# Kernel optimization log

Measured on AMD Instinct MI355X. Metric: run time of the kernel, lower is better.

Reference implementation:

```python
import jax, jax.numpy as jnp
import numpy as np

EPS_BN = 1e-5
NEG_SLOPE = 0.2

def _bn(x, gamma, beta):
    # BatchNorm1d using batch statistics (training-mode math, biased var as torch)
    mu = jnp.mean(x, axis=0)
    var = jnp.var(x, axis=0)
    return (x - mu) * jax.lax.rsqrt(var + EPS_BN) * gamma + beta

def _gat(x, src, dst, W, att_src, att_dst, bias, N):
    # x: [N, Fin]; W: [Fin, H*C]; att_*: [H, C]
    H, C = att_src.shape
    h = (x @ W).reshape(N, H, C)                       # [N,H,C]
    a_src = jnp.sum(h * att_src, axis=-1)              # [N,H]
    a_dst = jnp.sum(h * att_dst, axis=-1)              # [N,H]
    alpha = jax.nn.leaky_relu(a_src[src] + a_dst[dst], NEG_SLOPE)  # [E,H]
    # segment softmax over destination nodes
    m = jax.ops.segment_max(alpha, dst, num_segments=N)           # [N,H]
    e = jnp.exp(alpha - m[dst])
    s = jax.ops.segment_sum(e, dst, num_segments=N)
    a = e / (s[dst] + 1e-16)                           # [E,H]
    msg = h[src] * a[:, :, None]                       # [E,H,C]
    out = jax.ops.segment_sum(msg, dst, num_segments=N)  # [N,H,C]
    return out.reshape(N, H * C) + bias

def setup_inputs() -> dict:
    key = jax.random.key(0)
    ks = jax.random.split(key, 16)
    N, Fin, Hid = 50000, 128, 64
    E = 800000
    x = jax.random.normal(ks[0], (N, Fin), dtype=jnp.float32)
    edge_index = jax.random.randint(ks[1], (2, E), 0, N, dtype=jnp.int32)
    sc = 0.1
    return {
        'x': x,
        'edge_index': edge_index,
        'W1': jax.random.normal(ks[2], (Fin, 2 * Hid), jnp.float32) * sc,
        'att_src1': jax.random.normal(ks[3], (2, Hid), jnp.float32) * sc,
        'att_dst1': jax.random.normal(ks[4], (2, Hid), jnp.float32) * sc,
        'b1': jnp.zeros((2 * Hid,), jnp.float32),
        'g1': jnp.ones((2 * Hid,), jnp.float32),
        'be1': jnp.zeros((2 * Hid,), jnp.float32),
        'W2': jax.random.normal(ks[5], (2 * Hid, Hid), jnp.float32) * sc,
        'att_src2': jax.random.normal(ks[6], (1, Hid), jnp.float32) * sc,
        'att_dst2': jax.random.normal(ks[7], (1, Hid), jnp.float32) * sc,
        'b2': jnp.zeros((Hid,), jnp.float32),
        'g2': jnp.ones((Hid,), jnp.float32),
        'be2': jnp.zeros((Hid,), jnp.float32),
        'linW': jax.random.normal(ks[8], (Hid, 1), jnp.float32) * sc,
        'linb': jnp.zeros((1,), jnp.float32),
    }

def reference(x, edge_index, W1, att_src1, att_dst1, b1, g1, be1,
              W2, att_src2, att_dst2, b2, g2, be2, linW, linb):
    N = x.shape[0]
    loops = jnp.arange(N, dtype=edge_index.dtype)
    src = jnp.concatenate([edge_index[0], loops])  # PyG adds self-loops
    dst = jnp.concatenate([edge_index[1], loops])
    h = _gat(x, src, dst, W1, att_src1, att_dst1, b1, N)
    h = jax.nn.relu(_bn(h, g1, be1))                 # dropout = identity (eval)
    h = _gat(h, src, dst, W2, att_src2, att_dst2, b2, N)
    h = jax.nn.relu(_bn(h, g2, be2))
    return (h @ linW + linb).squeeze(-1)
```

## Files before the change

kernel.cpp:

```cpp
#include <hip/hip_runtime.h>
#include <hip/hip_fp16.h>
#include <math.h>

#define LEAKY 0.2f
#define XPAD 136
#define MAXB 512

typedef _Float16 f16x8 __attribute__((ext_vector_type(8)));
typedef float f32x4 __attribute__((ext_vector_type(4)));

__device__ inline int h2i(__half2 h) { union { __half2 h; int i; } u; u.h = h; return u.i; }
__device__ inline __half2 i2h(int i) { union { __half2 h; int i; } u; u.i = i; return u.h; }

__global__ __launch_bounds__(256) void k_bhist(const int* __restrict__ ei,
                                               int* __restrict__ gbcnt, int E, int PB)
{
  __shared__ int lh[MAXB];
  int t = threadIdx.x;
  for (int i = t; i < PB; i += 256) lh[i] = 0;
  __syncthreads();
  int base = blockIdx.x * 2048;
#pragma unroll
  for (int k = 0; k < 8; ++k) {
    int idx = base + t + k * 256;
    if (idx < E) atomicAdd(&lh[ei[E + idx] >> 7], 1);
  }
  __syncthreads();
  for (int i = t; i < PB; i += 256) if (lh[i]) atomicAdd(&gbcnt[i], lh[i]);
}

__global__ __launch_bounds__(512) void k_bscan(const int* __restrict__ gbcnt,
                                               int* __restrict__ pbase,
                                               int* __restrict__ gcur, int PB)
{
  __shared__ int ls[512];
  int t = threadIdx.x;
  int v = (t < PB) ? gbcnt[t] : 0;
  ls[t] = v;
  __syncthreads();
  for (int off = 1; off < 512; off <<= 1) {
    int u = (t >= off) ? ls[t - off] : 0;
    __syncthreads();
    ls[t] += u;
    __syncthreads();
  }
  int excl = ls[t] - v;
  if (t <= PB) pbase[t] = excl;
  if (t < PB) gcur[t] = excl;
}

__global__ __launch_bounds__(256) void k_part(const int* __restrict__ ei,
                                              int* __restrict__ gcur,
                                              int2* __restrict__ pairs, int E, int PB)
{
  __shared__ int lcnt[MAXB], lbase[MAXB];
  int t = threadIdx.x;
  for (int i = t; i < PB; i += 256) lcnt[i] = 0;
  __syncthreads();
  int base = blockIdx.x * 4096;
  int lsrc[16], ldst[16], lp[16];
#pragma unroll
  for (int k = 0; k < 16; ++k) {
    int idx = base + t + k * 256;
    lp[k] = -1;
    if (idx < E) {
      int s = ei[idx], d = ei[E + idx];
      lsrc[k] = s; ldst[k] = d;
      int b = d >> 7;
      int p = atomicAdd(&lcnt[b], 1);
      lp[k] = (p << 10) | b;
    }
  }
  __syncthreads();
  for (int b = t; b < PB; b += 256) lbase[b] = atomicAdd(&gcur[b], lcnt[b]);
  __syncthreads();
#pragma unroll
  for (int k = 0; k < 16; ++k) {
    if (lp[k] >= 0) {
      int b = lp[k] & 1023, p = lp[k] >> 10;
      pairs[lbase[b] + p] = make_int2(lsrc[k], ldst[k]);
    }
  }
}

__global__ __launch_bounds__(256) void k_fine(const int2* __restrict__ pairs,
                                              const int* __restrict__ pbase,
                                              int* __restrict__ rowptr,
                                              int* __restrict__ colx, int N)
{
  __shared__ int ldeg[128], lcur[128];
  int b = blockIdx.x, t = threadIdx.x;
  int nbase = b << 7;
  int nbn = N - nbase; if (nbn > 128) nbn = 128;
  if (t < 128) ldeg[t] = (t < nbn) ? 1 : 0;
  __syncthreads();
  int e0 = pbase[b], e1 = pbase[b + 1];
  for (int e = e0 + t; e < e1; e += 256) atomicAdd(&ldeg[pairs[e].y - nbase], 1);
  __syncthreads();
  int myv = (t < 128) ? ldeg[t] : 0;
  for (int off = 1; off < 128; off <<= 1) {
    int u = (t < 128 && t >= off) ? ldeg[t - off] : 0;
    __syncthreads();
    if (t < 128) ldeg[t] += u;
    __syncthreads();
  }
  int colx0 = e0 + nbase;
  if (t < 128) {
    int excl = ldeg[t] - myv;
    lcur[t] = colx0 + excl;
    int idx = nbase + t;
    if (idx <= N) rowptr[idx] = colx0 + excl;
  }
  __syncthreads();
  for (int e = e0 + t; e < e1; e += 256) {
    int2 p = pairs[e];
    int pos = atomicAdd(&lcur[p.y - nbase], 1);
    colx[pos] = p.x;
  }
  if (t < nbn) {
    int pos = atomicAdd(&lcur[t], 1);
    colx[pos] = nbase + t;
  }
}

__global__ __launch_bounds__(256) void k_gemm1(
    const float* __restrict__ x, const float* __restrict__ W,
    const float* __restrict__ att_s, const float* __restrict__ att_d,
    unsigned* __restrict__ h1h, float* __restrict__ a1s, float* __restrict__ a1d, int N)
{
  __shared__ __align__(16) _Float16 Xh[64 * XPAD];
  __shared__ __align__(16) _Float16 Wt[128 * XPAD];
  int t = threadIdx.x;
  const float4* W4 = (const float4*)W;
#pragma unroll
  for (int i = 0; i < 16; ++i) {
    int id = t + i * 256;
    int row = id >> 5, c0 = (id & 31) * 4;
    float4 wv = W4[id];
    Wt[(c0    ) * XPAD + row] = (_Float16)wv.x;
    Wt[(c0 + 1) * XPAD + row] = (_Float16)wv.y;
    Wt[(c0 + 2) * XPAD + row] = (_Float16)wv.z;
    Wt[(c0 + 3) * XPAD + row] = (_Float16)wv.w;
  }
  int row0 = blockIdx.x * 64;
  const float4* X4 = (const float4*)x;
#pragma unroll
  for (int i = 0; i < 8; ++i) {
    int id = t + i * 256;
    int r = id >> 5, c = id & 31;
    int gr = row0 + r;
    float4 v = (gr < N) ? X4[(size_t)gr * 32 + c] : make_float4(0.f, 0.f, 0.f, 0.f);
    unsigned p01 = (unsigned)h2i(__floats2half2_rn(v.x, v.y));
    unsigned p23 = (unsigned)h2i(__floats2half2_rn(v.z, v.w));
    *(uint2*)&Xh[r * XPAD + c * 4] = make_uint2(p01, p23);
  }
  __syncthreads();
  int w = t >> 6, l = t & 63;
  int m = l & 15, kg = l >> 4;
  f32x4 acc[8];
#pragma unroll
  for (int c = 0; c < 8; ++c) { acc[c][0] = 0.f; acc[c][1] = 0.f; acc[c][2] = 0.f; acc[c][3] = 0.f; }
#pragma unroll
  for (int ks = 0; ks < 4; ++ks) {
    f16x8 a = *(const f16x8*)&Xh[(w * 16 + m) * XPAD + ks * 32 + kg * 8];
#pragma unroll
    for (int c = 0; c < 8; ++c) {
      f16x8 bfr = *(const f16x8*)&Wt[(c * 16 + m) * XPAD + ks * 32 + kg * 8];
      acc[c] = __builtin_amdgcn_mfma_f32_16x16x32_f16(a, bfr, acc[c], 0, 0, 0);
    }
  }
#pragma unroll
  for (int c = 0; c < 8; ++c)
#pragma unroll
    for (int r = 0; r < 4; ++r)
      Xh[(w * 16 + kg * 4 + r) * XPAD + c * 16 + m] = (_Float16)acc[c][r];
  __syncthreads();
#pragma unroll
  for (int i = 0; i < 8; ++i) {
    int id = t + i * 256;
    int r = id >> 5, c4 = id & 31;
    int gr = row0 + r;
    uint2 pk = *(const uint2*)&Xh[r * XPAD + c4 * 4];
    float2 v01 = __half22float2(i2h((int)pk.x));
    float2 v23 = __half22float2(i2h((int)pk.y));
    int col = c4 * 4;
    float4 asv = *(const float4*)&att_s[col];
    float4 adv = *(const float4*)&att_d[col];
    float ps = v01.x * asv.x + v01.y * asv.y + v23.x * asv.z + v23.y * asv.w;
    float pd = v01.x * adv.x + v01.y * adv.y + v23.x * adv.z + v23.y * adv.w;
    ps += __shfl_xor(ps, 1); ps += __shfl_xor(ps, 2); ps += __shfl_xor(ps, 4); ps += __shfl_xor(ps, 8);
    pd += __shfl_xor(pd, 1); pd += __shfl_xor(pd, 2); pd += __shfl_xor(pd, 4); pd += __shfl_xor(pd, 8);
    if (gr < N) {
      *(uint2*)&h1h[(size_t)gr * 64 + c4 * 2] = pk;
      if ((t & 15) == 0) { int h = (t >> 4) & 1; a1s[gr * 2 + h] = ps; a1d[gr * 2 + h] = pd; }
    }
  }
}

__global__ __launch_bounds__(256) void k_agg1(
    const int* __restrict__ rowptr, const int* __restrict__ colx,
    const unsigned* __restrict__ h1h, const float* __restrict__ a1s,
    const float* __restrict__ a1d, const float* __restrict__ b1,
    unsigned* __restrict__ v1h, float* __restrict__ stats, int N)
{
  int t = threadIdx.x;
  int w = t >> 6, lane = t & 63;
  int g = lane >> 4, q = lane & 15;
  bool hi = q >= 8;
  int n = blockIdx.x * 16 + w * 4 + g;
  bool act = n < N;
  float4 biasA = *(const float4*)&b1[q * 8];
  float4 biasB = *(const float4*)&b1[q * 8 + 4];
  int start = 0, end = 0;
  float2 ad = make_float2(0.f, 0.f);
  if (act) { start = rowptr[n]; end = rowptr[n + 1]; ad = *(const float2*)&a1d[n * 2]; }
  float se = 0.f;
  float4 accA = {0, 0, 0, 0}, accB = {0, 0, 0, 0};
  for (int base = start; base < end; base += 16) {
    int cnt = end - base; if (cnt > 16) cnt = 16;
    int sl = 0, epk = 0;
    if (q < cnt) {
      sl = colx[base + q];
      float2 av = *(const float2*)&a1s[sl * 2];
      float x0 = av.x + ad.x, x1 = av.y + ad.y;
      x0 = (x0 > 0.f) ? x0 : LEAKY * x0;
      x1 = (x1 > 0.f) ? x1 : LEAKY * x1;
      epk = h2i(__floats2half2_rn(__expf(x0), __expf(x1)));
    }
    int j = 0;
    if (cnt == 16) {
      int ss[16], ee[16];
#pragma unroll
      for (int k = 0; k < 16; ++k) { ss[k] = __shfl(sl, k, 16); ee[k] = __shfl(epk, k, 16); }
      uint4 rr[16];
#pragma unroll
      for (int k = 0; k < 16; ++k) rr[k] = *(const uint4*)&h1h[(size_t)ss[k] * 64 + q * 4];
#pragma unroll
      for (int k = 0; k < 16; ++k) {
        float2 ef = __half22float2(i2h(ee[k]));
        float wg = hi ? ef.y : ef.x;
        float2 r0 = __half22float2(i2h((int)rr[k].x));
        float2 r1 = __half22float2(i2h((int)rr[k].y));
        float2 r2 = __half22float2(i2h((int)rr[k].z));
        float2 r3 = __half22float2(i2h((int)rr[k].w));
        se += wg;
        accA.x = fmaf(wg, r0.x, accA.x); accA.y = fmaf(wg, r0.y, accA.y);
        accA.z = fmaf(wg, r1.x, accA.z); accA.w = fmaf(wg, r1.y, accA.w);
        accB.x = fmaf(wg, r2.x, accB.x); accB.y = fmaf(wg, r2.y, accB.y);
        accB.z = fmaf(wg, r3.x, accB.z); accB.w = fmaf(wg, r3.y, accB.w);
      }
      j = 16;
    }
    int lim8 = cnt & ~7;
    for (; j < lim8; j += 8) {
      int ss[8], ee[8];
#pragma unroll
      for (int k = 0; k < 8; ++k) { ss[k] = __shfl(sl, j + k, 16); ee[k] = __shfl(epk, j + k, 16); }
      uint4 rr[8];
#pragma unroll
      for (int k = 0; k < 8; ++k) rr[k] = *(const uint4*)&h1h[(size_t)ss[k] * 64 + q * 4];
#pragma unroll
      for (int k = 0; k < 8; ++k) {
        float2 ef = __half22float2(i2h(ee[k]));
        float wg = hi ? ef.y : ef.x;
        float2 r0 = __half22float2(i2h((int)rr[k].x));
        float2 r1 = __half22float2(i2h((int)rr[k].y));
        float2 r2 = __half22float2(i2h((int)rr[k].z));
        float2 r3 = __half22float2(i2h((int)rr[k].w));
        se += wg;
        accA.x = fmaf(wg, r0.x, accA.x); accA.y = fmaf(wg, r0.y, accA.y);
        accA.z = fmaf(wg, r1.x, accA.z); accA.w = fmaf(wg, r1.y, accA.w);
        accB.x = fmaf(wg, r2.x, accB.x); accB.y = fmaf(wg, r2.y, accB.y);
        accB.z = fmaf(wg, r3.x, accB.z); accB.w = fmaf(wg, r3.y, accB.w);
      }
    }
    for (; j < cnt; ++j) {
      int s0 = __shfl(sl, j, 16), e0 = __shfl(epk, j, 16);
      float2 ef = __half22float2(i2h(e0));
      float wg = hi ? ef.y : ef.x;
      uint4 rv = *(const uint4*)&h1h[(size_t)s0 * 64 + q * 4];
      float2 r0 = __half22float2(i2h((int)rv.x));
      float2 r1 = __half22float2(i2h((int)rv.y));
      float2 r2 = __half22float2(i2h((int)rv.z));
      float2 r3 = __half22float2(i2h((int)rv.w));
      se += wg;
      accA.x = fmaf(wg, r0.x, accA.x); accA.y = fmaf(wg, r0.y, accA.y);
      accA.z = fmaf(wg, r1.x, accA.z); accA.w = fmaf(wg, r1.y, accA.w);
      accB.x = fmaf(wg, r2.x, accB.x); accB.y = fmaf(wg, r2.y, accB.y);
      accB.z = fmaf(wg, r3.x, accB.z); accB.w = fmaf(wg, r3.y, accB.w);
    }
  }
  float4 oA = {0,0,0,0}, oB = {0,0,0,0};
  if (act) {
    float inv = 1.f / se;
    oA.x = fmaf(accA.x, inv, biasA.x);
    oA.y = fmaf(accA.y, inv, biasA.y);
    oA.z = fmaf(accA.z, inv, biasA.z);
    oA.w = fmaf(accA.w, inv, biasA.w);
    oB.x = fmaf(accB.x, inv, biasB.x);
    oB.y = fmaf(accB.y, inv, biasB.y);
    oB.z = fmaf(accB.z, inv, biasB.z);
    oB.w = fmaf(accB.w, inv, biasB.w);
    unsigned p0 = (unsigned)h2i(__floats2half2_rn(oA.x, oA.y));
    unsigned p1 = (unsigned)h2i(__floats2half2_rn(oA.z, oA.w));
    unsigned p2 = (unsigned)h2i(__floats2half2_rn(oB.x, oB.y));
    unsigned p3 = (unsigned)h2i(__floats2half2_rn(oB.z, oB.w));
    *(uint4*)&v1h[(size_t)n * 64 + q * 4] = make_uint4(p0, p1, p2, p3);
  }
  __shared__ float redS[4][64][8], redQ[4][64][8];
#pragma unroll
  for (int j2 = 0; j2 < 4; ++j2) {
    redS[w][lane][j2]     = (&oA.x)[j2];
    redS[w][lane][4 + j2] = (&oB.x)[j2];
    redQ[w][lane][j2]     = (&oA.x)[j2] * (&oA.x)[j2];
    redQ[w][lane][4 + j2] = (&oB.x)[j2] * (&oB.x)[j2];
  }
  __syncthreads();
  if (t < 128) {
    int qq = t >> 3, jj = t & 7;
    float s = 0.f, sq = 0.f;
#pragma unroll
    for (int w2 = 0; w2 < 4; ++w2)
#pragma unroll
      for (int g2 = 0; g2 < 4; ++g2) {
        s  += redS[w2][g2 * 16 + qq][jj];
        sq += redQ[w2][g2 * 16 + qq][jj];
      }
    int sl8 = (blockIdx.x & 7) * 256;
    atomicAdd(&stats[sl8 + t], s);
    atomicAdd(&stats[sl8 + 128 + t], sq);
  }
}

__global__ __launch_bounds__(256) void k_gemm2(
    const unsigned* __restrict__ v1h, const float* __restrict__ W2,
    const float* __restrict__ stats, const float* __restrict__ g1, const float* __restrict__ be1,
    const float* __restrict__ att_s, const float* __restrict__ att_d,
    unsigned* __restrict__ h2h, float* __restrict__ a2s, float* __restrict__ a2d,
    int N, float rcpN)
{
  __shared__ __align__(16) _Float16 Xh[64 * XPAD];
  __shared__ __align__(16) _Float16 Wt[64 * XPAD];
  __shared__ float kc[128], sc[128];
  int t = threadIdx.x;
  if (t < 128) {
    float su = 0.f, sq = 0.f;
#pragma unroll
    for (int s8 = 0; s8 < 8; ++s8) { su += stats[s8 * 256 + t]; sq += stats[s8 * 256 + 128 + t]; }
    float mu = su * rcpN;
    float var = sq * rcpN - mu * mu;
    float kk = g1[t] * rsqrtf(var + 1e-5f);
    kc[t] = kk; sc[t] = be1[t] - mu * kk;
  }
  const float4* W4 = (const float4*)W2;
#pragma unroll
  for (int i = 0; i < 8; ++i) {
    int id = t + i * 256;
    int row = id >> 4, c0 = (id & 15) * 4;
    float4 wv = W4[id];
    Wt[(c0    ) * XPAD + row] = (_Float16)wv.x;
    Wt[(c0 + 1) * XPAD + row] = (_Float16)wv.y;
    Wt[(c0 + 2) * XPAD + row] = (_Float16)wv.z;
    Wt[(c0 + 3) * XPAD + row] = (_Float16)wv.w;
  }
  __syncthreads();
  int row0 = blockIdx.x * 64;
#pragma unroll
  for (int i = 0; i < 8; ++i) {
    int id = t + i * 256;
    int r = id >> 5, c4 = id & 31;
    int gr = row0 + r;
    uint2 pv = (gr < N) ? *(const uint2*)&v1h[(size_t)gr * 64 + c4 * 2] : make_uint2(0, 0);
    float2 a01 = __half22float2(i2h((int)pv.x));
    float2 a23 = __half22float2(i2h((int)pv.y));
    int f0 = c4 * 4;
    float o0 = fmaxf(a01.x * kc[f0]     + sc[f0],     0.f);
    float o1 = fmaxf(a01.y * kc[f0 + 1] + sc[f0 + 1], 0.f);
    float o2 = fmaxf(a23.x * kc[f0 + 2] + sc[f0 + 2], 0.f);
    float o3 = fmaxf(a23.y * kc[f0 + 3] + sc[f0 + 3], 0.f);
    unsigned p01 = (unsigned)h2i(__floats2half2_rn(o0, o1));
    unsigned p23 = (unsigned)h2i(__floats2half2_rn(o2, o3));
    *(uint2*)&Xh[r * XPAD + c4 * 4] = make_uint2(p01, p23);
  }
  __syncthreads();
  int w = t >> 6, l = t & 63;
  int m = l & 15, kg = l >> 4;
  f32x4 acc[4];
#pragma unroll
  for (int c = 0; c < 4; ++c) { acc[c][0] = 0.f; acc[c][1] = 0.f; acc[c][2] = 0.f; acc[c][3] = 0.f; }
#pragma unroll
  for (int ks = 0; ks < 4; ++ks) {
    f16x8 a = *(const f16x8*)&Xh[(w * 16 + m) * XPAD + ks * 32 + kg * 8];
#pragma unroll
    for (int c = 0; c < 4; ++c) {
      f16x8 bfr = *(const f16x8*)&Wt[(c * 16 + m) * XPAD + ks * 32 + kg * 8];
      acc[c] = __builtin_amdgcn_mfma_f32_16x16x32_f16(a, bfr, acc[c], 0, 0, 0);
    }
  }
#pragma unroll
  for (int c = 0; c < 4; ++c)
#pragma unroll
    for (int r = 0; r < 4; ++r)
      Xh[(w * 16 + kg * 4 + r) * XPAD + c * 16 + m] = (_Float16)acc[c][r];
  __syncthreads();
#pragma unroll
  for (int i = 0; i < 4; ++i) {
    int id = t + i * 256;
    int r = id >> 4, c4 = id & 15;
    int gr = row0 + r;
    uint2 pk = *(const uint2*)&Xh[r * XPAD + c4 * 4];
    float2 v01 = __half22float2(i2h((int)pk.x));
    float2 v23 = __half22float2(i2h((int)pk.y));
    int col = c4 * 4;
    float4 asv = *(const float4*)&att_s[col];
    float4 adv = *(const float4*)&att_d[col];
    float ps = v01.x * asv.x + v01.y * asv.y + v23.x * asv.z + v23.y * asv.w;
    float pd = v01.x * adv.x + v01.y * adv.y + v23.x * adv.z + v23.y * adv.w;
    ps += __shfl_xor(ps, 1); ps += __shfl_xor(ps, 2); ps += __shfl_xor(ps, 4); ps += __shfl_xor(ps, 8);
    pd += __shfl_xor(pd, 1); pd += __shfl_xor(pd, 2); pd += __shfl_xor(pd, 4); pd += __shfl_xor(pd, 8);
    if (gr < N) {
      *(uint2*)&h2h[(size_t)gr * 32 + c4 * 2] = pk;
      if ((t & 15) == 0) { a2s[gr] = ps; a2d[gr] = pd; }
    }
  }
}

__global__ __launch_bounds__(256) void k_agg2(
    const int* __restrict__ rowptr, const int* __restrict__ colx,
    const unsigned* __restrict__ h2h, const float* __restrict__ a2s,
    const float* __restrict__ a2d, const float* __restrict__ b2,
    unsigned* __restrict__ v2h, float* __restrict__ stats, int N)
{
  int t = threadIdx.x;
  int w = t >> 6, lane = t & 63;
  int g = lane >> 4, q = lane & 15;
  int n = blockIdx.x * 16 + w * 4 + g;
  bool act = n < N;
  float4 bias = *(const float4*)&b2[q * 4];
  int start = 0, end = 0;
  float ad = 0.f;
  if (act) { start = rowptr[n]; end = rowptr[n + 1]; ad = a2d[n]; }
  float se = 0.f;
  float4 acc = {0, 0, 0, 0};
  for (int base = start; base < end; base += 16) {
    int cnt = end - base; if (cnt > 16) cnt = 16;
    int sl = 0; float ev = 0.f;
    if (q < cnt) {
      sl = colx[base + q];
      float av = a2s[sl] + ad;
      av = (av > 0.f) ? av : LEAKY * av;
      ev = __expf(av);
    }
    int j = 0;
    if (cnt == 16) {
      int ss[16]; float ee[16];
#pragma unroll
      for (int k = 0; k < 16; ++k) { ss[k] = __shfl(sl, k, 16); ee[k] = __shfl(ev, k, 16); }
      uint2 rr[16];
#pragma unroll
      for (int k = 0; k < 16; ++k) rr[k] = *(const uint2*)&h2h[(size_t)ss[k] * 32 + q * 2];
#pragma unroll
      for (int k = 0; k < 16; ++k) {
        float2 r01 = __half22float2(i2h((int)rr[k].x));
        float2 r23 = __half22float2(i2h((int)rr[k].y));
        se += ee[k];
        acc.x = fmaf(ee[k], r01.x, acc.x);
        acc.y = fmaf(ee[k], r01.y, acc.y);
        acc.z = fmaf(ee[k], r23.x, acc.z);
        acc.w = fmaf(ee[k], r23.y, acc.w);
      }
      j = 16;
    }
    int lim8 = cnt & ~7;
    for (; j < lim8; j += 8) {
      int ss[8]; float ee[8];
#pragma unroll
      for (int k = 0; k < 8; ++k) { ss[k] = __shfl(sl, j + k, 16); ee[k] = __shfl(ev, j + k, 16); }
      uint2 rr[8];
#pragma unroll
      for (int k = 0; k < 8; ++k) rr[k] = *(const uint2*)&h2h[(size_t)ss[k] * 32 + q * 2];
#pragma unroll
      for (int k = 0; k < 8; ++k) {
        float2 r01 = __half22float2(i2h((int)rr[k].x));
        float2 r23 = __half22float2(i2h((int)rr[k].y));
        se += ee[k];
        acc.x = fmaf(ee[k], r01.x, acc.x);
        acc.y = fmaf(ee[k], r01.y, acc.y);
        acc.z = fmaf(ee[k], r23.x, acc.z);
        acc.w = fmaf(ee[k], r23.y, acc.w);
      }
    }
    for (; j < cnt; ++j) {
      int s0 = __shfl(sl, j, 16);
      float e0 = __shfl(ev, j, 16);
      uint2 rv = *(const uint2*)&h2h[(size_t)s0 * 32 + q * 2];
      float2 r01 = __half22float2(i2h((int)rv.x));
      float2 r23 = __half22float2(i2h((int)rv.y));
      se += e0;
      acc.x = fmaf(e0, r01.x, acc.x);
      acc.y = fmaf(e0, r01.y, acc.y);
      acc.z = fmaf(e0, r23.x, acc.z);
      acc.w = fmaf(e0, r23.y, acc.w);
    }
  }
  float4 o = {0, 0, 0, 0};
  if (act) {
    float inv = 1.f / se;
    o.x = fmaf(acc.x, inv, bias.x);
    o.y = fmaf(acc.y, inv, bias.y);
    o.z = fmaf(acc.z, inv, bias.z);
    o.w = fmaf(acc.w, inv, bias.w);
    unsigned p01 = (unsigned)h2i(__floats2half2_rn(o.x, o.y));
    unsigned p23 = (unsigned)h2i(__floats2half2_rn(o.z, o.w));
    *(uint2*)&v2h[(size_t)n * 32 + q * 2] = make_uint2(p01, p23);
  }
  __shared__ float4 reds[4][64], redq[4][64];
  reds[w][lane] = o;
  redq[w][lane] = make_float4(o.x * o.x, o.y * o.y, o.z * o.z, o.w * o.w);
  __syncthreads();
  if (t < 64) {
    int qq = t >> 2, ii = t & 3;
    float s = 0.f, sq = 0.f;
#pragma unroll
    for (int w2 = 0; w2 < 4; ++w2)
#pragma unroll
      for (int g2 = 0; g2 < 4; ++g2) {
        s  += (&reds[w2][g2 * 16 + qq].x)[ii];
        sq += (&redq[w2][g2 * 16 + qq].x)[ii];
      }
    int sl8 = (blockIdx.x & 7) * 128;
    atomicAdd(&stats[sl8 + t], s);
    atomicAdd(&stats[sl8 + 64 + t], sq);
  }
}

__global__ __launch_bounds__(256) void k_out(
    const unsigned* __restrict__ v2h, const float* __restrict__ stats,
    const float* __restrict__ g2, const float* __restrict__ be2,
    const float* __restrict__ linW, const float* __restrict__ linb,
    float* __restrict__ out, int N, float rcpN)
{
  __shared__ float kc[64], sc[64], lw[64];
  int t = threadIdx.x;
  if (t < 64) {
    float su = 0.f, sq = 0.f;
#pragma unroll
    for (int s8 = 0; s8 < 8; ++s8) { su += stats[s8 * 128 + t]; sq += stats[s8 * 128 + 64 + t]; }
    float mu = su * rcpN;
    float var = sq * rcpN - mu * mu;
    float kk = g2[t] * rsqrtf(var + 1e-5f);
    kc[t] = kk; sc[t] = be2[t] - mu * kk; lw[t] = linW[t];
  }
  __syncthreads();
  int w = t >> 6, lane = t & 63, g = lane >> 5, q = lane & 31;
  int n = blockIdx.x * 8 + w * 2 + g;
  if (n >= N) return;
  unsigned uv = v2h[(size_t)n * 32 + q];
  float2 vf = __half22float2(i2h((int)uv));
  float h0 = fmaxf(vf.x * kc[2 * q] + sc[2 * q], 0.f);
  float h1 = fmaxf(vf.y * kc[2 * q + 1] + sc[2 * q + 1], 0.f);
  float p = fmaf(h0, lw[2 * q], h1 * lw[2 * q + 1]);
#pragma unroll
  for (int off = 16; off; off >>= 1) p += __shfl_xor(p, off, 32);
  if (q == 0) out[n] = p + linb[0];
}

extern "C" void kernel_launch(void* const* d_in, const int* in_sizes, int n_in,
                              void* d_out, int out_size, void* d_ws, size_t ws_size,
                              hipStream_t stream)
{
  const float* x    = (const float*)d_in[0];
  const int*   ei   = (const int*)d_in[1];
  const float* W1   = (const float*)d_in[2];
  const float* as1  = (const float*)d_in[3];
  const float* ad1  = (const float*)d_in[4];
  const float* b1   = (const float*)d_in[5];
  const float* g1   = (const float*)d_in[6];
  const float* be1  = (const float*)d_in[7];
  const float* W2   = (const float*)d_in[8];
  const float* as2  = (const float*)d_in[9];
  const float* ad2  = (const float*)d_in[10];
  const float* b2   = (const float*)d_in[11];
  const float* g2   = (const float*)d_in[12];
  const float* be2  = (const float*)d_in[13];
  const float* linW = (const float*)d_in[14];
  const float* linb = (const float*)d_in[15];
  float* out = (float*)d_out;

  int N = in_sizes[0] / 128;
  int E = in_sizes[1] / 2;
  int Etot = E + N;
  float rcpN = 1.f / (float)N;
  int PB = (N + 127) / 128;

  float* ws = (float*)d_ws;
  size_t o = 0;
  float* H1HF = ws + o; o += (size_t)N * 64;
  float* V1HF = ws + o; o += (size_t)N * 64;
  float* A1S  = ws + o; o += (size_t)N * 2;
  float* A1D  = ws + o; o += (size_t)N * 2;
  float* A2S  = ws + o; o += N;
  float* A2D  = ws + o; o += N;
  float* ST1  = ws + o; o += 8 * 256;
  float* ST2  = ws + o; o += 8 * 128;
  int* GBCNT  = (int*)(ws + o); o += MAXB;
  int* PBASE  = (int*)(ws + o); o += MAXB + 1;
  int* GCUR   = (int*)(ws + o); o += MAXB;
  int* ROWPTR = (int*)(ws + o); o += (size_t)N + 1;
  int* COL    = (int*)(ws + o); o += (size_t)Etot;
  int2* PAIRS = (int2*)(ws + o); o += (size_t)E * 2;
  unsigned* H1H = (unsigned*)H1HF;
  unsigned* H2H = (unsigned*)H1HF;
  unsigned* V1H = (unsigned*)V1HF;
  unsigned* V2H = (unsigned*)V1HF;

  hipMemsetAsync(ST1, 0, (3072 + MAXB) * 4, stream);

  int gb  = (N + 63) / 64;
  int bh  = (E + 2047) / 2048;
  int pt  = (E + 4095) / 4096;
  int ab1 = (N + 15) / 16;
  int ab2 = (N + 15) / 16;
  int ob  = (N + 7) / 8;

  k_bhist<<<bh, 256, 0, stream>>>(ei, GBCNT, E, PB);
  k_bscan<<<1, 512, 0, stream>>>(GBCNT, PBASE, GCUR, PB);
  k_part<<<pt, 256, 0, stream>>>(ei, GCUR, PAIRS, E, PB);
  k_fine<<<PB, 256, 0, stream>>>(PAIRS, PBASE, ROWPTR, COL, N);
  k_gemm1<<<gb, 256, 0, stream>>>(x, W1, as1, ad1, H1H, A1S, A1D, N);
  k_agg1<<<ab1, 256, 0, stream>>>(ROWPTR, COL, H1H, A1S, A1D, b1, V1H, ST1, N);
  k_gemm2<<<gb, 256, 0, stream>>>(V1H, W2, ST1, g1, be1, as2, ad2, H2H, A2S, A2D, N, rcpN);
  k_agg2<<<ab2, 256, 0, stream>>>(ROWPTR, COL, H2H, A2S, A2D, b2, V2H, ST2, N);
  k_out<<<ob, 256, 0, stream>>>(V2H, ST2, g2, be2, linW, linb, out, N, rcpN);
}
```

Before: 167.2 us.

## Fold bucket scan into partition kernels and widen layer-2 aggregation vectors

Removes the single-block k_bscan launch by having every k_part block redundantly scan the bucket counts. k_fine now derives its edge range with a block-level reduction over the preceding counts, and GCUR becomes a zero-based offset cleared by the enlarged memset. k_agg2 switches to 8 lanes per node with 16-byte gathers, 8 channels per lane and 32 nodes per block, and the reduction buffers get padding to avoid LDS bank conflicts. This saves a launch and a serial dependency, but adds redundant scan work in every partition and fine block.

```diff
diff --git a/kernel.cpp b/kernel.cpp
--- a/kernel.cpp
+++ b/kernel.cpp
@@ -29,50 +29,44 @@
   for (int i = t; i < PB; i += 256) if (lh[i]) atomicAdd(&gbcnt[i], lh[i]);
 }
 
-__global__ __launch_bounds__(512) void k_bscan(const int* __restrict__ gbcnt,
-                                               int* __restrict__ pbase,
-                                               int* __restrict__ gcur, int PB)
-{
-  __shared__ int ls[512];
+__global__ __launch_bounds__(256) void k_part(const int* __restrict__ ei,
+                                              const int* __restrict__ gbcnt,
+                                              int* __restrict__ gcur,
+                                              int2* __restrict__ pairs, int E, int PB)
+{
+  __shared__ int lcnt[MAXB], lpb[MAXB], lbase[MAXB], ls[256];
   int t = threadIdx.x;
-  int v = (t < PB) ? gbcnt[t] : 0;
-  ls[t] = v;
-  __syncthreads();
-  for (int off = 1; off < 512; off <<= 1) {
+  for (int i = t; i < PB; i += 256) lcnt[i] = 0;
+  int ea = (2 * t < PB) ? gbcnt[2 * t] : 0;
+  int eb = (2 * t + 1 < PB) ? gbcnt[2 * t + 1] : 0;
+  int s = ea + eb;
+  ls[t] = s;
+  __syncthreads();
+  int base = blockIdx.x * 4096;
+  int lsrc[16], ldst[16], lp[16];
+#pragma unroll
+  for (int k = 0; k < 16; ++k) {
+    int idx = base + t + k * 256;
+    lp[k] = -1;
+    if (idx < E) {
+      int sv = ei[idx], dv = ei[E + idx];
+      lsrc[k] = sv; ldst[k] = dv;
+      int b = dv >> 7;
+      int p = atomicAdd(&lcnt[b], 1);
+      lp[k] = (p << 10) | b;
+    }
+  }
+  for (int off = 1; off < 256; off <<= 1) {
     int u = (t >= off) ? ls[t - off] : 0;
     __syncthreads();
     ls[t] += u;
     __syncthreads();
   }
-  int excl = ls[t] - v;
-  if (t <= PB) pbase[t] = excl;
-  if (t < PB) gcur[t] = excl;
-}
-
-__global__ __launch_bounds__(256) void k_part(const int* __restrict__ ei,
-                                              int* __restrict__ gcur,
-                                              int2* __restrict__ pairs, int E, int PB)
-{
-  __shared__ int lcnt[MAXB], lbase[MAXB];
-  int t = threadIdx.x;
-  for (int i = t; i < PB; i += 256) lcnt[i] = 0;
-  __syncthreads();
-  int base = blockIdx.x * 4096;
-  int lsrc[16], ldst[16], lp[16];
-#pragma unroll
-  for (int k = 0; k < 16; ++k) {
-    int idx = base + t + k * 256;
-    lp[k] = -1;
-    if (idx < E) {
-      int s = ei[idx], d = ei[E + idx];
-      lsrc[k] = s; ldst[k] = d;
-      int b = d >> 7;
-      int p = atomicAdd(&lcnt[b], 1);
-      lp[k] = (p << 10) | b;
-    }
-  }
-  __syncthreads();
-  for (int b = t; b < PB; b += 256) lbase[b] = atomicAdd(&gcur[b], lcnt[b]);
+  int excl = ls[t] - s;
+  if (2 * t < MAXB) lpb[2 * t] = excl;
+  if (2 * t + 1 < MAXB) lpb[2 * t + 1] = excl + ea;
+  __syncthreads();
+  for (int b = t; b < PB; b += 256) lbase[b] = lpb[b] + atomicAdd(&gcur[b], lcnt[b]);
   __syncthreads();
 #pragma unroll
   for (int k = 0; k < 16; ++k) {
@@ -84,17 +78,25 @@
 }
 
 __global__ __launch_bounds__(256) void k_fine(const int2* __restrict__ pairs,
-                                              const int* __restrict__ pbase,
+                                              const int* __restrict__ gbcnt,
                                               int* __restrict__ rowptr,
                                               int* __restrict__ colx, int N)
 {
-  __shared__ int ldeg[128], lcur[128];
+  __shared__ int ldeg[128], lcur[128], lred[256];
   int b = blockIdx.x, t = threadIdx.x;
   int nbase = b << 7;
   int nbn = N - nbase; if (nbn > 128) nbn = 128;
+  int part = 0;
+  for (int i = t; i < b; i += 256) part += gbcnt[i];
+  lred[t] = part;
   if (t < 128) ldeg[t] = (t < nbn) ? 1 : 0;
   __syncthreads();
-  int e0 = pbase[b], e1 = pbase[b + 1];
+  for (int off = 128; off; off >>= 1) {
+    if (t < off) lred[t] += lred[t + off];
+    __syncthreads();
+  }
+  int e0 = lred[0];
+  int e1 = e0 + gbcnt[b];
   for (int e = e0 + t; e < e1; e += 256) atomicAdd(&ldeg[pairs[e].y - nbase], 1);
   __syncthreads();
   int myv = (t < 128) ? ldeg[t] : 0;
@@ -307,7 +309,7 @@
     unsigned p3 = (unsigned)h2i(__floats2half2_rn(oB.z, oB.w));
     *(uint4*)&v1h[(size_t)n * 64 + q * 4] = make_uint4(p0, p1, p2, p3);
   }
-  __shared__ float redS[4][64][8], redQ[4][64][8];
+  __shared__ float redS[4][64][9], redQ[4][64][9];
 #pragma unroll
   for (int j2 = 0; j2 < 4; ++j2) {
     redS[w][lane][j2]     = (&oA.x)[j2];
@@ -433,17 +435,18 @@
 {
   int t = threadIdx.x;
   int w = t >> 6, lane = t & 63;
-  int g = lane >> 4, q = lane & 15;
-  int n = blockIdx.x * 16 + w * 4 + g;
+  int g = lane >> 3, q = lane & 7;
+  int n = blockIdx.x * 32 + w * 8 + g;
   bool act = n < N;
-  float4 bias = *(const float4*)&b2[q * 4];
+  float4 biasA = *(const float4*)&b2[q * 8];
+  float4 biasB = *(const float4*)&b2[q * 8 + 4];
   int start = 0, end = 0;
   float ad = 0.f;
   if (act) { start = rowptr[n]; end = rowptr[n + 1]; ad = a2d[n]; }
   float se = 0.f;
-  float4 acc = {0, 0, 0, 0};
-  for (int base = start; base < end; base += 16) {
-    int cnt = end - base; if (cnt > 16) cnt = 16;
+  float4 accA = {0, 0, 0, 0}, accB = {0, 0, 0, 0};
+  for (int base = start; base < end; base += 8) {
+    int cnt = end - base; if (cnt > 8) cnt = 8;
     int sl = 0; float ev = 0.f;
     if (q < cnt) {
       sl = colx[base + q];
@@ -452,81 +455,98 @@
       ev = __expf(av);
     }
     int j = 0;
-    if (cnt == 16) {
-      int ss[16]; float ee[16];
-#pragma unroll
-      for (int k = 0; k < 16; ++k) { ss[k] = __shfl(sl, k, 16); ee[k] = __shfl(ev, k, 16); }
-      uint2 rr[16];
-#pragma unroll
-      for (int k = 0; k < 16; ++k) rr[k] = *(const uint2*)&h2h[(size_t)ss[k] * 32 + q * 2];
-#pragma unroll
-      for (int k = 0; k < 16; ++k) {
-        float2 r01 = __half22float2(i2h((int)rr[k].x));
-        float2 r23 = __half22float2(i2h((int)rr[k].y));
+    if (cnt == 8) {
+      int ss[8]; float ee[8];
+#pragma unroll
+      for (int k = 0; k < 8; ++k) { ss[k] = __shfl(sl, k, 8); ee[k] = __shfl(ev, k, 8); }
+      uint4 rr[8];
+#pragma unroll
+      for (int k = 0; k < 8; ++k) rr[k] = *(const uint4*)&h2h[(size_t)ss[k] * 32 + q * 4];
+#pragma unroll
+      for (int k = 0; k < 8; ++k) {
+        float2 r0 = __half22float2(i2h((int)rr[k].x));
+        float2 r1 = __half22float2(i2h((int)rr[k].y));
+        float2 r2 = __half22float2(i2h((int)rr[k].z));
+        float2 r3 = __half22float2(i2h((int)rr[k].w));
         se += ee[k];
-        acc.x = fmaf(ee[k], r01.x, acc.x);
-        acc.y = fmaf(ee[k], r01.y, acc.y);
-        acc.z = fmaf(ee[k], r23.x, acc.z);
-        acc.w = fmaf(ee[k], r23.y, acc.w);
+        accA.x = fmaf(ee[k], r0.x, accA.x); accA.y = fmaf(ee[k], r0.y, accA.y);
+        accA.z = fmaf(ee[k], r1.x, accA.z); accA.w = fmaf(ee[k], r1.y, accA.w);
+        accB.x = fmaf(ee[k], r2.x, accB.x); accB.y = fmaf(ee[k], r2.y, accB.y);
+        accB.z = fmaf(ee[k], r3.x, accB.z); accB.w = fmaf(ee[k], r3.y, accB.w);
       }
-      j = 16;
-    }
-    int lim8 = cnt & ~7;
-    for (; j < lim8; j += 8) {
-      int ss[8]; float ee[8];
-#pragma unroll
-      for (int k = 0; k < 8; ++k) { ss[k] = __shfl(sl, j + k, 16); ee[k] = __shfl(ev, j + k, 16); }
-      uint2 rr[8];
-#pragma unroll
-      for (int k = 0; k < 8; ++k) rr[k] = *(const uint2*)&h2h[(size_t)ss[k] * 32 + q * 2];
-#pragma unroll
-      for (int k = 0; k < 8; ++k) {
-        float2 r01 = __half22float2(i2h((int)rr[k].x));
-        float2 r23 = __half22float2(i2h((int)rr[k].y));
+      j = 8;
+    }
+    int lim4 = cnt & ~3;
+    for (; j < lim4; j += 4) {
+      int ss[4]; float ee[4];
+#pragma unroll
+      for (int k = 0; k < 4; ++k) { ss[k] = __shfl(sl, j + k, 8); ee[k] = __shfl(ev, j + k, 8); }
+      uint4 rr[4];
+#pragma unroll
+      for (int k = 0; k < 4; ++k) rr[k] = *(const uint4*)&h2h[(size_t)ss[k] * 32 + q * 4];
+#pragma unroll
+      for (int k = 0; k < 4; ++k) {
+        float2 r0 = __half22float2(i2h((int)rr[k].x));
+        float2 r1 = __half22float2(i2h((int)rr[k].y));
+        float2 r2 = __half22float2(i2h((int)rr[k].z));
+        float2 r3 = __half22float2(i2h((int)rr[k].w));
         se += ee[k];
-        acc.x = fmaf(ee[k], r01.x, acc.x);
-        acc.y = fmaf(ee[k], r01.y, acc.y);
-        acc.z = fmaf(ee[k], r23.x, acc.z);
-        acc.w = fmaf(ee[k], r23.y, acc.w);
+        accA.x = fmaf(ee[k], r0.x, accA.x); accA.y = fmaf(ee[k], r0.y, accA.y);
+        accA.z = fmaf(ee[k], r1.x, accA.z); accA.w = fmaf(ee[k], r1.y, accA.w);
+        accB.x = fmaf(ee[k], r2.x, accB.x); accB.y = fmaf(ee[k], r2.y, accB.y);
+        accB.z = fmaf(ee[k], r3.x, accB.z); accB.w = fmaf(ee[k], r3.y, accB.w);
       }
     }
     for (; j < cnt; ++j) {
-      int s0 = __shfl(sl, j, 16);
-      float e0 = __shfl(ev, j, 16);
-      uint2 rv = *(const uint2*)&h2h[(size_t)s0 * 32 + q * 2];
-      float2 r01 = __half22float2(i2h((int)rv.x));
-      float2 r23 = __half22float2(i2h((int)rv.y));
+      int s0 = __shfl(sl, j, 8);
+      float e0 = __shfl(ev, j, 8);
+      uint4 rv = *(const uint4*)&h2h[(size_t)s0 * 32 + q * 4];
+      float2 r0 = __half22float2(i2h((int)rv.x));
+      float2 r1 = __half22float2(i2h((int)rv.y));
+      float2 r2 = __half22float2(i2h((int)rv.z));
+      float2 r3 = __half22float2(i2h((int)rv.w));
       se += e0;
-      acc.x = fmaf(e0, r01.x, acc.x);
-      acc.y = fmaf(e0, r01.y, acc.y);
-      acc.z = fmaf(e0, r23.x, acc.z);
-      acc.w = fmaf(e0, r23.y, acc.w);
-    }
-  }
-  float4 o = {0, 0, 0, 0};
+      accA.x = fmaf(e0, r0.x, accA.x); accA.y = fmaf(e0, r0.y, accA.y);
+      accA.z = fmaf(e0, r1.x, accA.z); accA.w = fmaf(e0, r1.y, accA.w);
+      accB.x = fmaf(e0, r2.x, accB.x); accB.y = fmaf(e0, r2.y, accB.y);
+      accB.z = fmaf(e0, r3.x, accB.z); accB.w = fmaf(e0, r3.y, accB.w);
+    }
+  }
+  float4 oA = {0,0,0,0}, oB = {0,0,0,0};
   if (act) {
     float inv = 1.f / se;
-    o.x = fmaf(acc.x, inv, bias.x);
-    o.y = fmaf(acc.y, inv, bias.y);
-    o.z = fmaf(acc.z, inv, bias.z);
-    o.w = fmaf(acc.w, inv, bias.w);
-    unsigned p01 = (unsigned)h2i(__floats2half2_rn(o.x, o.y));
-    unsigned p23 = (unsigned)h2i(__floats2half2_rn(o.z, o.w));
-    *(uint2*)&v2h[(size_t)n * 32 + q * 2] = make_uint2(p01, p23);
-  }
-  __shared__ float4 reds[4][64], redq[4][64];
-  reds[w][lane] = o;
-  redq[w][lane] = make_float4(o.x * o.x, o.y * o.y, o.z * o.z, o.w * o.w);
+    oA.x = fmaf(accA.x, inv, biasA.x);
+    oA.y = fmaf(accA.y, inv, biasA.y);
+    oA.z = fmaf(accA.z, inv, biasA.z);
+    oA.w = fmaf(accA.w, inv, biasA.w);
+    oB.x = fmaf(accB.x, inv, biasB.x);
+    oB.y = fmaf(accB.y, inv, biasB.y);
+    oB.z = fmaf(accB.z, inv, biasB.z);
+    oB.w = fmaf(accB.w, inv, biasB.w);
+    unsigned p0 = (unsigned)h2i(__floats2half2_rn(oA.x, oA.y));
+    unsigned p1 = (unsigned)h2i(__floats2half2_rn(oA.z, oA.w));
+    unsigned p2 = (unsigned)h2i(__floats2half2_rn(oB.x, oB.y));
+    unsigned p3 = (unsigned)h2i(__floats2half2_rn(oB.z, oB.w));
+    *(uint4*)&v2h[(size_t)n * 32 + q * 4] = make_uint4(p0, p1, p2, p3);
+  }
+  __shared__ float redS[4][64][9], redQ[4][64][9];
+#pragma unroll
+  for (int j2 = 0; j2 < 4; ++j2) {
+    redS[w][lane][j2]     = (&oA.x)[j2];
+    redS[w][lane][4 + j2] = (&oB.x)[j2];
+    redQ[w][lane][j2]     = (&oA.x)[j2] * (&oA.x)[j2];
+    redQ[w][lane][4 + j2] = (&oB.x)[j2] * (&oB.x)[j2];
+  }
   __syncthreads();
   if (t < 64) {
-    int qq = t >> 2, ii = t & 3;
+    int qq = t >> 3, jj = t & 7;
     float s = 0.f, sq = 0.f;
 #pragma unroll
     for (int w2 = 0; w2 < 4; ++w2)
 #pragma unroll
-      for (int g2 = 0; g2 < 4; ++g2) {
-        s  += (&reds[w2][g2 * 16 + qq].x)[ii];
-        sq += (&redq[w2][g2 * 16 + qq].x)[ii];
+      for (int g2 = 0; g2 < 8; ++g2) {
+        s  += redS[w2][g2 * 8 + qq][jj];
+        sq += redQ[w2][g2 * 8 + qq][jj];
       }
     int sl8 = (blockIdx.x & 7) * 128;
     atomicAdd(&stats[sl8 + t], s);
@@ -604,7 +624,6 @@
   float* ST1  = ws + o; o += 8 * 256;
   float* ST2  = ws + o; o += 8 * 128;
   int* GBCNT  = (int*)(ws + o); o += MAXB;
-  int* PBASE  = (int*)(ws + o); o += MAXB + 1;
   int* GCUR   = (int*)(ws + o); o += MAXB;
   int* ROWPTR = (int*)(ws + o); o += (size_t)N + 1;
   int* COL    = (int*)(ws + o); o += (size_t)Etot;
@@ -614,19 +633,18 @@
   unsigned* V1H = (unsigned*)V1HF;
   unsigned* V2H = (unsigned*)V1HF;
 
-  hipMemsetAsync(ST1, 0, (3072 + MAXB) * 4, stream);
+  hipMemsetAsync(ST1, 0, (3072 + 2 * MAXB) * 4, stream);
 
   int gb  = (N + 63) / 64;
   int bh  = (E + 2047) / 2048;
   int pt  = (E + 4095) / 4096;
   int ab1 = (N + 15) / 16;
-  int ab2 = (N + 15) / 16;
+  int ab2 = (N + 31) / 32;
   int ob  = (N + 7) / 8;
 
   k_bhist<<<bh, 256, 0, stream>>>(ei, GBCNT, E, PB);
-  k_bscan<<<1, 512, 0, stream>>>(GBCNT, PBASE, GCUR, PB);
-  k_part<<<pt, 256, 0, stream>>>(ei, GCUR, PAIRS, E, PB);
-  k_fine<<<PB, 256, 0, stream>>>(PAIRS, PBASE, ROWPTR, COL, N);
+  k_part<<<pt, 256, 0, stream>>>(ei, GBCNT, GCUR, PAIRS, E, PB);
+  k_fine<<<PB, 256, 0, stream>>>(PAIRS, GBCNT, ROWPTR, COL, N);
   k_gemm1<<<gb, 256, 0, stream>>>(x, W1, as1, ad1, H1H, A1S, A1D, N);
   k_agg1<<<ab1, 256, 0, stream>>>(ROWPTR, COL, H1H, A1S, A1D, b1, V1H, ST1, N);
   k_gemm2<<<gb, 256, 0, stream>>>(V1H, W2, ST1, g1, be1, as2, ad2, H2H, A2S, A2D, N, rcpN);
```

Result: faster. 158.4 us (-5.3%).
